# Kernel tuning notes

Measured on AMD Instinct MI355X. Metric: run time of the kernel, lower is better.

The kernel has to match this reference:

```python
import jax, jax.numpy as jnp
import numpy as np

N = 50000      # nodes
E = 800000     # edges (avg degree 16)
H = 128        # hidden_dim
GDIM = 64      # global feature dim
G = 10         # DiffGroupNorm groups
LAMDA = 0.01
EPS = 1e-5


def setup_inputs() -> dict:
    key = jax.random.key(0)
    ks = jax.random.split(key, 24)
    s = 0.05
    inp = {
        "x": jax.random.normal(ks[0], (N, H), dtype=jnp.float32),
        "edge_index": jax.random.randint(ks[1], (2, E), 0, N, dtype=jnp.int32),
        "edge_features": jax.random.normal(ks[2], (E, H), dtype=jnp.float32),
        "global_feat": jax.random.normal(ks[3], (1, GDIM), dtype=jnp.float32),
        # combine: Dense(H) on concat [x | messages | global] -> (H+H+GDIM, H)
        "Wc": jax.random.normal(ks[4], (H + H + GDIM, H), dtype=jnp.float32) * s,
        "bc": jnp.zeros((H,), jnp.float32),
    }
    for i, tag in enumerate(["a", "b"]):
        k = jax.random.split(ks[5 + i], 4)
        inp[f"W1{tag}"] = jax.random.normal(k[0], (H, H), dtype=jnp.float32) * s
        inp[f"b1{tag}"] = jnp.zeros((H,), jnp.float32)
        inp[f"W2{tag}"] = jax.random.normal(k[1], (H, H), dtype=jnp.float32) * s
        inp[f"b2{tag}"] = jnp.zeros((H,), jnp.float32)
        inp[f"linW{tag}"] = jax.random.normal(k[2], (H, G), dtype=jnp.float32) * s
        inp[f"linb{tag}"] = jnp.zeros((G,), jnp.float32)
        inp[f"gamma{tag}"] = jnp.ones((G * H,), jnp.float32)
        inp[f"beta{tag}"] = jnp.zeros((G * H,), jnp.float32)
    return inp


def _diff_group_norm(x, linW, linb, gamma, beta):
    # DiffGroupNorm: soft group assignment + per-(group,channel) batch norm.
    n, f = x.shape
    s = jax.nn.softmax(x @ linW + linb, axis=-1)            # [N, G]
    o = (s[:, :, None] * x[:, None, :]).reshape(n, G * f)   # [N, G*F]
    mu = o.mean(axis=0)
    var = o.var(axis=0)
    o = (o - mu) * jax.lax.rsqrt(var + EPS) * gamma + beta
    return x + LAMDA * o.reshape(n, G, f).sum(axis=1)


def _block(out, W1, b1, W2, b2, linW, linb, gamma, beta):
    h = jax.nn.softplus(out @ W1 + b1) @ W2 + b2
    h = _diff_group_norm(h, linW, linb, gamma, beta)
    return out + h


def reference(x, edge_index, edge_features, global_feat, Wc, bc,
              W1a, b1a, W2a, b2a, linWa, linba, gammaa, betaa,
              W1b, b1b, W2b, b2b, linWb, linbb, gammab, betab):
    n = x.shape[0]
    row = edge_index[0]
    # tf.scatter_nd accumulates duplicates -> segment sum over destination nodes
    messages = jax.ops.segment_sum(edge_features, row, num_segments=n)
    g = jnp.repeat(global_feat, n // global_feat.shape[0], axis=0)
    combined = jnp.concatenate([x, messages, g], axis=-1)
    out = jax.nn.softplus(combined @ Wc + bc)
    initial = out
    out = _block(out, W1a, b1a, W2a, b2a, linWa, linba, gammaa, betaa)
    out = _block(out, W1b, b1b, W2b, b2b, linWb, linbb, gammab, betab)
    return out + initial
```

## Files before the change

kernel.cpp:

```cpp
#include <hip/hip_runtime.h>
#include <math.h>

constexpr int NN = 50000;
constexpr int NE = 800000;
constexpr int HD = 128;
constexpr int NG = 10;
constexpr float LAM = 0.01f;
constexpr float EPSV = 1e-5f;
constexpr int NBLK = (NN + 255) / 256;
constexpr int GBLK = (NN + 63) / 64;
constexpr int NCOPY = 8;

typedef __attribute__((ext_vector_type(8))) short s8v;
typedef __attribute__((ext_vector_type(4))) float f4v;

constexpr int SMEM_BYTES = 76864;

__device__ __forceinline__ float softplus_f(float x) {
    return fmaxf(x, 0.f) + log1pf(expf(-fabsf(x)));
}
__device__ __forceinline__ unsigned short f2b(float f) {
    unsigned u = __float_as_uint(f);
    unsigned r = (u + 0x7FFFu + ((u >> 16) & 1u)) >> 16;
    return (unsigned short)r;
}
__device__ __forceinline__ float b2f(unsigned short u) {
    return __uint_as_float(((unsigned)u) << 16);
}

constexpr int EBLOCKS = (NE / 4 + 255) / 256;
__global__ __launch_bounds__(256) void hist_prep_kernel(
    const int* __restrict__ rows, int* __restrict__ cnt,
    const float* __restrict__ Wc,
    const float* __restrict__ W1a, const float* __restrict__ W2a,
    const float* __restrict__ W1b, const float* __restrict__ W2b,
    short* __restrict__ wct, short* __restrict__ wts)
{
    if ((int)blockIdx.x < EBLOCKS) {
        int base = (blockIdx.x * 256 + threadIdx.x) * 4;
        if (base < NE) {
            int4 r = *reinterpret_cast<const int4*>(rows + base);
            atomicAdd(&cnt[r.x], 1);
            atomicAdd(&cnt[r.y], 1);
            atomicAdd(&cnt[r.z], 1);
            atomicAdd(&cnt[r.w], 1);
        }
    } else {
        int i = (blockIdx.x - EBLOCKS) * 256 + threadIdx.x;
        if (i < 40960) {
            int n = i / 320, kk = i % 320;
            wct[i] = (short)f2b(Wc[kk * 128 + n]);
        } else if (i < 40960 + 4 * 16384) {
            int j = i - 40960;
            int mat = j >> 14;
            int idx = j & 16383;
            int n = idx >> 7, kk = idx & 127;
            const float* src = (mat == 0) ? W1a : (mat == 1) ? W2a
                             : (mat == 2) ? W1b : W2b;
            wts[j] = (short)f2b(src[kk * 128 + n]);
        }
    }
}

__global__ __launch_bounds__(256) void scan1_kernel(
    const int* __restrict__ cnt, int* __restrict__ bsum)
{
    __shared__ int red[256];
    int t = threadIdx.x;
    int i = blockIdx.x * 256 + t;
    red[t] = (i < NN) ? cnt[i] : 0;
    __syncthreads();
    for (int d = 128; d > 0; d >>= 1) {
        if (t < d) red[t] += red[t + d];
        __syncthreads();
    }
    if (t == 0) bsum[blockIdx.x] = red[0];
}

__global__ __launch_bounds__(256) void scan3_kernel(
    const int* __restrict__ cnt, const int* __restrict__ bsum,
    int* __restrict__ off, int* __restrict__ cur)
{
    __shared__ int sh[256];
    __shared__ int bs[256];
    __shared__ int basev;
    int t = threadIdx.x;
    int i = blockIdx.x * 256 + t;
    int v  = (i < NN) ? cnt[i] : 0;
    int bv = (t < NBLK) ? bsum[t] : 0;
    sh[t] = v; bs[t] = bv;
    __syncthreads();
    for (int d = 1; d < 256; d <<= 1) {
        int u1 = (t >= d) ? sh[t - d] : 0;
        int u2 = (t >= d) ? bs[t - d] : 0;
        __syncthreads();
        sh[t] += u1; bs[t] += u2;
        __syncthreads();
    }
    if (t == (int)blockIdx.x) basev = bs[t] - bv;
    __syncthreads();
    int excl = sh[t] - v + basev;
    if (i < NN) { off[i] = excl; cur[i] = excl; }
    if (i == NN - 1) off[NN] = NE;
}

__global__ __launch_bounds__(256) void fill_kernel(
    const int* __restrict__ rows, int* __restrict__ cur, int* __restrict__ eid)
{
    int base = (blockIdx.x * 256 + threadIdx.x) * 4;
    if (base < NE) {
        int4 r = *reinterpret_cast<const int4*>(rows + base);
        eid[atomicAdd(&cur[r.x], 1)] = base + 0;
        eid[atomicAdd(&cur[r.y], 1)] = base + 1;
        eid[atomicAdd(&cur[r.z], 1)] = base + 2;
        eid[atomicAdd(&cur[r.w], 1)] = base + 3;
    }
}

__global__ __launch_bounds__(256) void gather_kernel(
    const float* __restrict__ ef, const int* __restrict__ off,
    const int* __restrict__ eid, uint4* __restrict__ msgbf)
{
    int node = blockIdx.x * 4 + (threadIdx.x >> 6);
    if (node >= NN) return;
    int lane = threadIdx.x & 63;
    int eg = lane >> 4;
    int lc = lane & 15;
    int b = off[node], e = off[node + 1];
    float acc[8];
    #pragma unroll
    for (int j = 0; j < 8; ++j) acc[j] = 0.f;
    for (int i = b + eg; i < e; i += 4) {
        int ed = eid[i];
        const float* src = ef + (size_t)ed * HD + lc * 8;
        float4 v0 = *reinterpret_cast<const float4*>(src);
        float4 v1 = *reinterpret_cast<const float4*>(src + 4);
        acc[0] += v0.x; acc[1] += v0.y; acc[2] += v0.z; acc[3] += v0.w;
        acc[4] += v1.x; acc[5] += v1.y; acc[6] += v1.z; acc[7] += v1.w;
    }
    #pragma unroll
    for (int j = 0; j < 8; ++j) {
        acc[j] += __shfl_xor(acc[j], 16);
        acc[j] += __shfl_xor(acc[j], 32);
    }
    if (eg == 0) {
        uint4 pk;
        pk.x = (unsigned)f2b(acc[0]) | ((unsigned)f2b(acc[1]) << 16);
        pk.y = (unsigned)f2b(acc[2]) | ((unsigned)f2b(acc[3]) << 16);
        pk.z = (unsigned)f2b(acc[4]) | ((unsigned)f2b(acc[5]) << 16);
        pk.w = (unsigned)f2b(acc[6]) | ((unsigned)f2b(acc[7]) << 16);
        msgbf[(size_t)node * 16 + lc] = pk;
    }
}

__device__ __forceinline__ void fused12_tail(
    char* smem, const short* __restrict__ w2t,
    unsigned short* __restrict__ hbf, float* __restrict__ sout,
    float* __restrict__ sums_base, int m0)
{
    short* As = (short*)(smem);
    short* Ws = (short*)(smem + 17408);
    short* Ts = (short*)(smem + 52224);
    float* b1s = (float*)(smem + 69632);
    float* b2s = (float*)(smem + 70144);
    float* lws = (float*)(smem + 70656);
    float* lbs = (float*)(smem + 76288);
    float* hF = (float*)(smem);
    float* sS = (float*)(smem + 33792);

    const int tid = threadIdx.x;
    const int lane = tid & 63;
    const int wv = tid >> 6;
    const int fr = lane & 15;
    const int fc = lane >> 4;

    f4v acc[8];
    #pragma unroll
    for (int ct = 0; ct < 8; ++ct) acc[ct] = (f4v){0.f, 0.f, 0.f, 0.f};
    {
        const short* ap = As + (wv * 16 + fr) * 136 + fc * 8;
        const short* bp = Ws + fr * 136 + fc * 8;
        #pragma unroll
        for (int ks = 0; ks < 4; ++ks) {
            s8v a = *(const s8v*)(ap + ks * 32);
            #pragma unroll
            for (int ct = 0; ct < 8; ++ct) {
                s8v b = *(const s8v*)(bp + ct * 16 * 136 + ks * 32);
                acc[ct] = __builtin_amdgcn_mfma_f32_16x16x32_bf16(a, b, acc[ct], 0, 0, 0);
            }
        }
    }
    {
        int rb = wv * 16 + fc * 4;
        #pragma unroll
        for (int ct = 0; ct < 8; ++ct) {
            int col = ct * 16 + fr;
            float bv = b1s[col];
            #pragma unroll
            for (int r = 0; r < 4; ++r)
                Ts[(rb + r) * 136 + col] = (short)f2b(softplus_f(acc[ct][r] + bv));
        }
    }
    __syncthreads();
    {
        int col = tid >> 1, seg = (tid & 1) * 64;
        const short* src = w2t + (size_t)col * 128 + seg;
        #pragma unroll
        for (int j = 0; j < 8; ++j)
            *(s8v*)&Ws[col * 136 + seg + 8 * j] = *(const s8v*)(src + 8 * j);
    }
    __syncthreads();

    #pragma unroll
    for (int ct = 0; ct < 8; ++ct) acc[ct] = (f4v){0.f, 0.f, 0.f, 0.f};
    {
        const short* ap = Ts + (wv * 16 + fr) * 136 + fc * 8;
        const short* bp = Ws + fr * 136 + fc * 8;
        #pragma unroll
        for (int ks = 0; ks < 4; ++ks) {
            s8v a = *(const s8v*)(ap + ks * 32);
            #pragma unroll
            for (int ct = 0; ct < 8; ++ct) {
                s8v b = *(const s8v*)(bp + ct * 16 * 136 + ks * 32);
                acc[ct] = __builtin_amdgcn_mfma_f32_16x16x32_bf16(a, b, acc[ct], 0, 0, 0);
            }
        }
    }
    #pragma unroll
    for (int ct = 0; ct < 8; ++ct) {
        float bv = b2s[ct * 16 + fr];
        #pragma unroll
        for (int r = 0; r < 4; ++r) acc[ct][r] += bv;
    }
    float dot[4][10];
    #pragma unroll
    for (int r = 0; r < 4; ++r)
        #pragma unroll
        for (int g = 0; g < 10; ++g) dot[r][g] = 0.f;
    #pragma unroll
    for (int ct = 0; ct < 8; ++ct) {
        #pragma unroll
        for (int g = 0; g < 10; ++g) {
            float lwv = lws[(ct * 16 + fr) * 11 + g];
            #pragma unroll
            for (int r = 0; r < 4; ++r) dot[r][g] += acc[ct][r] * lwv;
        }
    }
    #pragma unroll
    for (int r = 0; r < 4; ++r)
        #pragma unroll
        for (int g = 0; g < 10; ++g) {
            float v = dot[r][g];
            v += __shfl_xor(v, 1);
            v += __shfl_xor(v, 2);
            v += __shfl_xor(v, 4);
            v += __shfl_xor(v, 8);
            dot[r][g] = v + lbs[g];
        }
    #pragma unroll
    for (int r = 0; r < 4; ++r) {
        float m = dot[r][0];
        #pragma unroll
        for (int g = 1; g < 10; ++g) m = fmaxf(m, dot[r][g]);
        float sum = 0.f;
        #pragma unroll
        for (int g = 0; g < 10; ++g) { dot[r][g] = expf(dot[r][g] - m); sum += dot[r][g]; }
        float inv = 1.f / sum;
        #pragma unroll
        for (int g = 0; g < 10; ++g) dot[r][g] *= inv;
    }
    const int growb = m0 + wv * 16 + fc * 4;
    const int rlocb = wv * 16 + fc * 4;
    unsigned short hq[8][4];
    #pragma unroll
    for (int ct = 0; ct < 8; ++ct) {
        int col = ct * 16 + fr;
        #pragma unroll
        for (int r = 0; r < 4; ++r) {
            hq[ct][r] = f2b(acc[ct][r]);
            int row = growb + r;
            if (row < NN) hbf[(size_t)row * 128 + col] = hq[ct][r];
        }
    }
    if (fr < 10) {
        #pragma unroll
        for (int r = 0; r < 4; ++r) {
            int row = growb + r;
            if (row < NN) {
                float v = 0.f;
                #pragma unroll
                for (int g = 0; g < 10; ++g) v = (fr == g) ? dot[r][g] : v;
                sout[(size_t)row * 10 + fr] = v;
            }
        }
    }
    __syncthreads();
    #pragma unroll
    for (int ct = 0; ct < 8; ++ct) {
        int col = ct * 16 + fr;
        #pragma unroll
        for (int r = 0; r < 4; ++r) {
            bool valid = (growb + r) < NN;
            hF[(rlocb + r) * 132 + col] = valid ? b2f(hq[ct][r]) : 0.f;
        }
    }
    if (fr < 10) {
        #pragma unroll
        for (int r = 0; r < 4; ++r) {
            bool valid = (growb + r) < NN;
            float v = 0.f;
            #pragma unroll
            for (int g = 0; g < 10; ++g) v = (fr == g) ? dot[r][g] : v;
            sS[(rlocb + r) * 10 + fr] = valid ? v : 0.f;
        }
    }
    __syncthreads();
    {
        float* sums = sums_base + (size_t)(blockIdx.x & (NCOPY - 1)) * 2560;
        const int c = tid & 127;
        const int g0 = (tid >> 7) * 5;
        float a1[5], a2[5];
        #pragma unroll
        for (int q = 0; q < 5; ++q) { a1[q] = 0.f; a2[q] = 0.f; }
        for (int n = 0; n < 64; ++n) {
            float hv = hF[n * 132 + c];
            #pragma unroll
            for (int q = 0; q < 5; ++q) {
                float pv = sS[n * 10 + g0 + q] * hv;
                a1[q] += pv;
                a2[q] += pv * pv;
            }
        }
        #pragma unroll
        for (int q = 0; q < 5; ++q) {
            atomicAdd(&sums[(g0 + q) * 128 + c], a1[q]);
            atomicAdd(&sums[1280 + (g0 + q) * 128 + c], a2[q]);
        }
    }
}

__global__ __launch_bounds__(256) void combine_f12a_kernel(
    const float* __restrict__ x, const short* __restrict__ msgbf,
    const float* __restrict__ gf, const short* __restrict__ wct,
    const float* __restrict__ bc,
    const short* __restrict__ w1t, const short* __restrict__ w2t,
    const float* __restrict__ b1, const float* __restrict__ b2,
    const float* __restrict__ linW, const float* __restrict__ linb,
    unsigned short* __restrict__ out0bf, unsigned short* __restrict__ hbf,
    float* __restrict__ sout, float* __restrict__ sums)
{
    __shared__ __align__(16) char smem[SMEM_BYTES];
    short* cAs = (short*)(smem);
    short* cWs = (short*)(smem + 9216);
    short* As  = (short*)(smem);
    short* Ws  = (short*)(smem + 17408);
    float* b1s = (float*)(smem + 69632);
    float* b2s = (float*)(smem + 70144);
    float* lws = (float*)(smem + 70656);
    float* lbs = (float*)(smem + 76288);
    float* bcs = (float*)(smem + 76352);

    const int tid = threadIdx.x;
    const int m0 = blockIdx.x * 64;
    if (tid < 128) { bcs[tid] = bc[tid]; b1s[tid] = b1[tid]; b2s[tid] = b2[tid]; }
    for (int i = tid; i < 1280; i += 256) lws[(i / 10) * 11 + (i % 10)] = linW[i];
    if (tid < 10) lbs[tid] = linb[tid];
    const int lane = tid & 63;
    const int wv = tid >> 6;
    const int fr = lane & 15;
    const int fc = lane >> 4;

    f4v acc[8];
    #pragma unroll
    for (int ct = 0; ct < 8; ++ct) acc[ct] = (f4v){0.f, 0.f, 0.f, 0.f};

    const int arow = tid >> 2;
    const int aseg = (tid & 3) * 16;
    const int wcol = tid >> 1;
    const int wseg = (tid & 1) * 32;

    for (int c = 0; c < 5; ++c) {
        const int k0 = c * 64;
        {
            short tmp[16];
            int grow = m0 + arow;
            if (grow >= NN) {
                #pragma unroll
                for (int j = 0; j < 16; ++j) tmp[j] = 0;
            } else if (c < 2) {
                const float* src = x + (size_t)grow * 128 + k0 + aseg;
                #pragma unroll
                for (int q = 0; q < 4; ++q) {
                    float4 v = *reinterpret_cast<const float4*>(src + 4 * q);
                    tmp[4*q+0] = (short)f2b(v.x); tmp[4*q+1] = (short)f2b(v.y);
                    tmp[4*q+2] = (short)f2b(v.z); tmp[4*q+3] = (short)f2b(v.w);
                }
            } else if (c < 4) {
                const short* src = msgbf + (size_t)grow * 128 + (k0 - 128) + aseg;
                *(s8v*)tmp = *(const s8v*)src;
                *(s8v*)(tmp + 8) = *(const s8v*)(src + 8);
            } else {
                const float* src = gf + aseg;
                #pragma unroll
                for (int q = 0; q < 4; ++q) {
                    float4 v = *reinterpret_cast<const float4*>(src + 4 * q);
                    tmp[4*q+0] = (short)f2b(v.x); tmp[4*q+1] = (short)f2b(v.y);
                    tmp[4*q+2] = (short)f2b(v.z); tmp[4*q+3] = (short)f2b(v.w);
                }
            }
            *(s8v*)&cAs[arow * 72 + aseg] = *(s8v*)tmp;
            *(s8v*)&cAs[arow * 72 + aseg + 8] = *(s8v*)(tmp + 8);
        }
        {
            const short* src = wct + (size_t)wcol * 320 + k0 + wseg;
            #pragma unroll
            for (int j = 0; j < 4; ++j)
                *(s8v*)&cWs[wcol * 72 + wseg + 8 * j] = *(const s8v*)(src + 8 * j);
        }
        __syncthreads();
        const short* ap = cAs + (wv * 16 + fr) * 72 + fc * 8;
        const short* bp = cWs + fr * 72 + fc * 8;
        #pragma unroll
        for (int ks = 0; ks < 2; ++ks) {
            s8v a = *(const s8v*)(ap + ks * 32);
            #pragma unroll
            for (int ct = 0; ct < 8; ++ct) {
                s8v b = *(const s8v*)(bp + ct * 16 * 72 + ks * 32);
                acc[ct] = __builtin_amdgcn_mfma_f32_16x16x32_bf16(a, b, acc[ct], 0, 0, 0);
            }
        }
        __syncthreads();
    }
    const int rbase = m0 + wv * 16 + fc * 4;
    const int rloc  = wv * 16 + fc * 4;
    #pragma unroll
    for (int ct = 0; ct < 8; ++ct) {
        int col = ct * 16 + fr;
        float bv = bcs[col];
        #pragma unroll
        for (int r = 0; r < 4; ++r) {
            unsigned short q = f2b(softplus_f(acc[ct][r] + bv));
            bool valid = (rbase + r) < NN;
            if (valid) out0bf[(size_t)(rbase + r) * 128 + col] = q;
            As[(rloc + r) * 136 + col] = valid ? (short)q : (short)0;
        }
    }
    {
        int col = tid >> 1, seg = (tid & 1) * 64;
        const short* src = w1t + (size_t)col * 128 + seg;
        #pragma unroll
        for (int j = 0; j < 8; ++j)
            *(s8v*)&Ws[col * 136 + seg + 8 * j] = *(const s8v*)(src + 8 * j);
    }
    __syncthreads();
    fused12_tail(smem, w2t, hbf, sout, sums, m0);
}

__global__ __launch_bounds__(256) void apply_f12b_kernel(
    const unsigned short* __restrict__ out0bf,
    const float* __restrict__ sums_a,
    const float* __restrict__ gamma_a, const float* __restrict__ beta_a,
    const short* __restrict__ w1t, const short* __restrict__ w2t,
    const float* __restrict__ b1, const float* __restrict__ b2,
    const float* __restrict__ linW, const float* __restrict__ linb,
    unsigned short* __restrict__ out1bf,
    unsigned short* __restrict__ hbf,
    float* __restrict__ sout,
    float* __restrict__ sums_b)
{
    __shared__ __align__(16) char smem[SMEM_BYTES];
    float* ws_  = (float*)(smem);
    float* mus_ = (float*)(smem + 5120);
    float* ks_  = (float*)(smem + 10240);
    float* ss_  = (float*)(smem + 10752);
    short* As   = (short*)(smem);
    short* Ws   = (short*)(smem + 17408);
    float* b1s  = (float*)(smem + 69632);
    float* b2s  = (float*)(smem + 70144);
    float* lws  = (float*)(smem + 70656);
    float* lbs  = (float*)(smem + 76288);

    const int tid = threadIdx.x;
    const int m0 = blockIdx.x * 64;
    if (tid < 128) { b1s[tid] = b1[tid]; b2s[tid] = b2[tid]; }
    for (int i = tid; i < 1280; i += 256) lws[(i / 10) * 11 + (i % 10)] = linW[i];
    if (tid < 10) lbs[tid] = linb[tid];
    const float invn = 1.f / (float)NN;
    for (int idx = tid; idx < 1280; idx += 256) {
        float s1 = 0.f, s2 = 0.f;
        #pragma unroll
        for (int k = 0; k < NCOPY; ++k) {
            s1 += sums_a[(size_t)k * 2560 + idx];
            s2 += sums_a[(size_t)k * 2560 + idx + 1280];
        }
        float mu = s1 * invn;
        float var = s2 * invn - mu * mu;
        float wg = rsqrtf(var + EPSV) * gamma_a[idx];
        ws_[idx] = wg;
        mus_[idx] = mu;
    }
    for (int i = tid; i < 640; i += 256) {
        int n = m0 + i / 10;
        ss_[i] = (n < NN) ? sout[(size_t)n * 10 + i % 10] : 0.f;
    }
    {
        int col = tid >> 1, seg = (tid & 1) * 64;
        const short* src = w1t + (size_t)col * 128 + seg;
        #pragma unroll
        for (int j = 0; j < 8; ++j)
            *(s8v*)&Ws[col * 136 + seg + 8 * j] = *(const s8v*)(src + 8 * j);
    }
    __syncthreads();
    if (tid < 128) {
        float kacc = 0.f;
        #pragma unroll
        for (int g = 0; g < NG; ++g) {
            int idx = g * 128 + tid;
            kacc += beta_a[idx] - mus_[idx] * ws_[idx];
        }
        ks_[tid] = kacc;
    }
    __syncthreads();
    const int tc = tid & 31, rg = tid >> 5;
    ushort4 vals[8];
    #pragma unroll
    for (int p = 0; p < 8; ++p) {
        int nl = p * 8 + rg;
        int n = m0 + nl;
        if (n >= NN) { vals[p].x = vals[p].y = vals[p].z = vals[p].w = 0; continue; }
        float A0 = 0.f, A1 = 0.f, A2 = 0.f, A3 = 0.f;
        #pragma unroll
        for (int g = 0; g < 10; ++g) {
            float sv = ss_[nl * 10 + g];
            float4 wv4 = *reinterpret_cast<const float4*>(&ws_[g * 128 + tc * 4]);
            A0 += sv * wv4.x; A1 += sv * wv4.y; A2 += sv * wv4.z; A3 += sv * wv4.w;
        }
        ushort4 hv4 = *reinterpret_cast<const ushort4*>(hbf + (size_t)n * 128 + tc * 4);
        ushort4 ov4 = *reinterpret_cast<const ushort4*>(out0bf + (size_t)n * 128 + tc * 4);
        float h0 = b2f(hv4.x), h1 = b2f(hv4.y), h2 = b2f(hv4.z), h3 = b2f(hv4.w);
        float r0 = b2f(ov4.x) + h0 + LAM * (h0 * A0 + ks_[tc * 4 + 0]);
        float r1 = b2f(ov4.y) + h1 + LAM * (h1 * A1 + ks_[tc * 4 + 1]);
        float r2 = b2f(ov4.z) + h2 + LAM * (h2 * A2 + ks_[tc * 4 + 2]);
        float r3 = b2f(ov4.w) + h3 + LAM * (h3 * A3 + ks_[tc * 4 + 3]);
        ushort4 o;
        o.x = f2b(r0); o.y = f2b(r1); o.z = f2b(r2); o.w = f2b(r3);
        *reinterpret_cast<ushort4*>(out1bf + (size_t)n * 128 + tc * 4) = o;
        vals[p] = o;
    }
    __syncthreads();
    #pragma unroll
    for (int p = 0; p < 8; ++p) {
        int row = p * 8 + rg;
        *reinterpret_cast<ushort4*>(&As[row * 136 + tc * 4]) = vals[p];
    }
    __syncthreads();
    fused12_tail(smem, w2t, hbf, sout, sums_b, m0);
}

__global__ __launch_bounds__(256) void apply_last_kernel(
    const unsigned short* __restrict__ out1bf,
    const unsigned short* __restrict__ hbf,
    const float* __restrict__ s, const float* __restrict__ sums,
    const float* __restrict__ gamma, const float* __restrict__ beta,
    const unsigned short* __restrict__ out0bf,
    float* __restrict__ dstf)
{
    __shared__ __align__(16) float ws_[1280];
    __shared__ float mus_[1280];
    __shared__ float ks_[128];
    __shared__ float ss_[640];
    const int tid = threadIdx.x;
    const int m0 = blockIdx.x * 64;
    const float invn = 1.f / (float)NN;
    for (int idx = tid; idx < 1280; idx += 256) {
        float s1 = 0.f, s2 = 0.f;
        #pragma unroll
        for (int k = 0; k < NCOPY; ++k) {
            s1 += sums[(size_t)k * 2560 + idx];
            s2 += sums[(size_t)k * 2560 + idx + 1280];
        }
        float mu = s1 * invn;
        float var = s2 * invn - mu * mu;
        float wg = rsqrtf(var + EPSV) * gamma[idx];
        ws_[idx] = wg;
        mus_[idx] = mu;
    }
    for (int i = tid; i < 640; i += 256) {
        int n = m0 + i / 10;
        ss_[i] = (n < NN) ? s[(size_t)n * 10 + i % 10] : 0.f;
    }
    __syncthreads();
    if (tid < 128) {
        float kacc = 0.f;
        #pragma unroll
        for (int g = 0; g < NG; ++g) {
            int idx = g * 128 + tid;
            kacc += beta[idx] - mus_[idx] * ws_[idx];
        }
        ks_[tid] = kacc;
    }
    __syncthreads();
    const int tc = tid & 31, rg = tid >> 5;
    #pragma unroll
    for (int p = 0; p < 8; ++p) {
        int nl = p * 8 + rg;
        int n = m0 + nl;
        if (n >= NN) continue;
        float A0 = 0.f, A1 = 0.f, A2 = 0.f, A3 = 0.f;
        #pragma unroll
        for (int g = 0; g < 10; ++g) {
            float sv = ss_[nl * 10 + g];
            float4 wv4 = *reinterpret_cast<const float4*>(&ws_[g * 128 + tc * 4]);
            A0 += sv * wv4.x; A1 += sv * wv4.y; A2 += sv * wv4.z; A3 += sv * wv4.w;
        }
        ushort4 hv4 = *reinterpret_cast<const ushort4*>(hbf + (size_t)n * 128 + tc * 4);
        ushort4 ov4 = *reinterpret_cast<const ushort4*>(out1bf + (size_t)n * 128 + tc * 4);
        ushort4 iv4 = *reinterpret_cast<const ushort4*>(out0bf + (size_t)n * 128 + tc * 4);
        float h0 = b2f(hv4.x), h1 = b2f(hv4.y), h2 = b2f(hv4.z), h3 = b2f(hv4.w);
        float r0 = b2f(ov4.x) + h0 + LAM * (h0 * A0 + ks_[tc * 4 + 0]) + b2f(iv4.x);
        float r1 = b2f(ov4.y) + h1 + LAM * (h1 * A1 + ks_[tc * 4 + 1]) + b2f(iv4.y);
        float r2 = b2f(ov4.z) + h2 + LAM * (h2 * A2 + ks_[tc * 4 + 2]) + b2f(iv4.z);
        float r3 = b2f(ov4.w) + h3 + LAM * (h3 * A3 + ks_[tc * 4 + 3]) + b2f(iv4.w);
        *reinterpret_cast<float4*>(dstf + (size_t)n * 128 + tc * 4) =
            make_float4(r0, r1, r2, r3);
    }
}

extern "C" void kernel_launch(void* const* d_in, const int* in_sizes, int n_in,
                              void* d_out, int out_size, void* d_ws, size_t ws_size,
                              hipStream_t stream)
{
    const float* x    = (const float*)d_in[0];
    const int*   eidx = (const int*)  d_in[1];
    const float* ef   = (const float*)d_in[2];
    const float* gf   = (const float*)d_in[3];
    const float* Wc   = (const float*)d_in[4];
    const float* bc   = (const float*)d_in[5];

    float* p = (float*)d_ws;
    int*   cnt    = (int*)p;                      p += NN;
    float* sums_a = p;                            p += (size_t)NCOPY * 2560;
    float* sums_b = p;                            p += (size_t)NCOPY * 2560;
    unsigned short* msgbf  = (unsigned short*)p;  p += (size_t)NN * 64;
    unsigned short* out0bf = (unsigned short*)p;  p += (size_t)NN * 64;
    unsigned short* out1bf = (unsigned short*)p;  p += (size_t)NN * 64;
    unsigned short* hbf    = (unsigned short*)p;  p += (size_t)NN * 64;
    float* sbuf = p;                              p += (size_t)NN * 10;
    short* wct  = (short*)p;
    short* wts  = wct + 40960;

    int* off   = (int*)out1bf;
    int* cur   = off + NN + 1;
    int* bsum  = cur + NN;
    int* eid   = (int*)hbf;

    hipMemsetAsync(cnt, 0, sizeof(int) * (NN + 2 * NCOPY * 2560), stream);

    hist_prep_kernel<<<EBLOCKS + 416, 256, 0, stream>>>(
        eidx, cnt, Wc, (const float*)d_in[6], (const float*)d_in[8],
        (const float*)d_in[14], (const float*)d_in[16], wct, wts);

    scan1_kernel<<<NBLK, 256, 0, stream>>>(cnt, bsum);
    scan3_kernel<<<NBLK, 256, 0, stream>>>(cnt, bsum, off, cur);
    fill_kernel <<<EBLOCKS, 256, 0, stream>>>(eidx, cur, eid);
    gather_kernel<<<(NN + 3) / 4, 256, 0, stream>>>(ef, off, eid, (uint4*)msgbf);

    const short* w1ta = wts;
    const short* w2ta = wts + 16384;
    const short* w1tb = wts + 32768;
    const short* w2tb = wts + 49152;

    combine_f12a_kernel<<<GBLK, 256, 0, stream>>>(
        x, (const short*)msgbf, gf, wct, bc,
        w1ta, w2ta, (const float*)d_in[7], (const float*)d_in[9],
        (const float*)d_in[10], (const float*)d_in[11],
        out0bf, hbf, sbuf, sums_a);

    apply_f12b_kernel<<<GBLK, 256, 0, stream>>>(
        out0bf, sums_a, (const float*)d_in[12], (const float*)d_in[13],
        w1tb, w2tb, (const float*)d_in[15], (const float*)d_in[17],
        (const float*)d_in[18], (const float*)d_in[19],
        out1bf, hbf, sbuf, sums_b);

    apply_last_kernel<<<GBLK, 256, 0, stream>>>(
        out1bf, hbf, sbuf, sums_b, (const float*)d_in[20], (const float*)d_in[21],
        out0bf, (float*)d_out);
}
```

Measured before the change: 397.3 us.

## Merge CSR build and gather front-end into one cooperative kernel

```diff
diff --git a/kernel.cpp b/kernel.cpp
--- a/kernel.cpp
+++ b/kernel.cpp
@@ -1,5 +1,8 @@
 #include <hip/hip_runtime.h>
+#include <hip/hip_cooperative_groups.h>
 #include <math.h>
+
+namespace cg = cooperative_groups;
 
 constexpr int NN = 50000;
 constexpr int NE = 800000;
@@ -10,6 +13,7 @@
 constexpr int NBLK = (NN + 255) / 256;
 constexpr int GBLK = (NN + 63) / 64;
 constexpr int NCOPY = 8;
+constexpr int FGRID = 1024;
 
 typedef __attribute__((ext_vector_type(8))) short s8v;
 typedef __attribute__((ext_vector_type(4))) float f4v;
@@ -28,128 +32,128 @@
     return __uint_as_float(((unsigned)u) << 16);
 }
 
-constexpr int EBLOCKS = (NE / 4 + 255) / 256;
-__global__ __launch_bounds__(256) void hist_prep_kernel(
-    const int* __restrict__ rows, int* __restrict__ cnt,
+__global__ __launch_bounds__(256) void frontend_kernel(
+    const int* __restrict__ rows,
+    int* __restrict__ zbase, int zcount,
+    int* __restrict__ cnt, int* __restrict__ bsum,
+    int* __restrict__ off, int* __restrict__ cur, int* __restrict__ eid,
+    const float* __restrict__ ef, uint4* __restrict__ msgbf,
+    const float* __restrict__ x, unsigned short* __restrict__ xbf,
     const float* __restrict__ Wc,
     const float* __restrict__ W1a, const float* __restrict__ W2a,
     const float* __restrict__ W1b, const float* __restrict__ W2b,
     short* __restrict__ wct, short* __restrict__ wts)
 {
-    if ((int)blockIdx.x < EBLOCKS) {
-        int base = (blockIdx.x * 256 + threadIdx.x) * 4;
-        if (base < NE) {
-            int4 r = *reinterpret_cast<const int4*>(rows + base);
-            atomicAdd(&cnt[r.x], 1);
-            atomicAdd(&cnt[r.y], 1);
-            atomicAdd(&cnt[r.z], 1);
-            atomicAdd(&cnt[r.w], 1);
-        }
-    } else {
-        int i = (blockIdx.x - EBLOCKS) * 256 + threadIdx.x;
-        if (i < 40960) {
-            int n = i / 320, kk = i % 320;
-            wct[i] = (short)f2b(Wc[kk * 128 + n]);
-        } else if (i < 40960 + 4 * 16384) {
-            int j = i - 40960;
-            int mat = j >> 14;
-            int idx = j & 16383;
-            int n = idx >> 7, kk = idx & 127;
-            const float* src = (mat == 0) ? W1a : (mat == 1) ? W2a
-                             : (mat == 2) ? W1b : W2b;
-            wts[j] = (short)f2b(src[kk * 128 + n]);
-        }
-    }
-}
-
-__global__ __launch_bounds__(256) void scan1_kernel(
-    const int* __restrict__ cnt, int* __restrict__ bsum)
-{
-    __shared__ int red[256];
-    int t = threadIdx.x;
-    int i = blockIdx.x * 256 + t;
-    red[t] = (i < NN) ? cnt[i] : 0;
-    __syncthreads();
-    for (int d = 128; d > 0; d >>= 1) {
-        if (t < d) red[t] += red[t + d];
+    cg::grid_group grid = cg::this_grid();
+    __shared__ int sA[256];
+    __shared__ int sB[256];
+    __shared__ int basev;
+    const int t = threadIdx.x;
+    const int gtid = blockIdx.x * 256 + t;
+    const int nthr = gridDim.x * 256;
+
+    for (int i = gtid; i < zcount; i += nthr) zbase[i] = 0;
+    for (int i = gtid; i < 40960; i += nthr) {
+        int n = i / 320, kk = i % 320;
+        wct[i] = (short)f2b(Wc[kk * 128 + n]);
+    }
+    for (int j = gtid; j < 65536; j += nthr) {
+        int mat = j >> 14, idx = j & 16383;
+        int n = idx >> 7, kk = idx & 127;
+        const float* src = (mat == 0) ? W1a : (mat == 1) ? W2a
+                         : (mat == 2) ? W1b : W2b;
+        wts[j] = (short)f2b(src[kk * 128 + n]);
+    }
+    for (int i = gtid; i < NN * 32; i += nthr) {
+        float4 v = reinterpret_cast<const float4*>(x)[i];
+        ushort4 o;
+        o.x = f2b(v.x); o.y = f2b(v.y); o.z = f2b(v.z); o.w = f2b(v.w);
+        reinterpret_cast<ushort4*>(xbf)[i] = o;
+    }
+    grid.sync();
+
+    for (int i = gtid; i < NE / 4; i += nthr) {
+        int4 r = reinterpret_cast<const int4*>(rows)[i];
+        atomicAdd(&cnt[r.x], 1);
+        atomicAdd(&cnt[r.y], 1);
+        atomicAdd(&cnt[r.z], 1);
+        atomicAdd(&cnt[r.w], 1);
+    }
+    grid.sync();
+
+    if ((int)blockIdx.x < NBLK) {
+        int i = blockIdx.x * 256 + t;
+        sA[t] = (i < NN) ? cnt[i] : 0;
         __syncthreads();
-    }
-    if (t == 0) bsum[blockIdx.x] = red[0];
-}
-
-__global__ __launch_bounds__(256) void scan3_kernel(
-    const int* __restrict__ cnt, const int* __restrict__ bsum,
-    int* __restrict__ off, int* __restrict__ cur)
-{
-    __shared__ int sh[256];
-    __shared__ int bs[256];
-    __shared__ int basev;
-    int t = threadIdx.x;
-    int i = blockIdx.x * 256 + t;
-    int v  = (i < NN) ? cnt[i] : 0;
-    int bv = (t < NBLK) ? bsum[t] : 0;
-    sh[t] = v; bs[t] = bv;
-    __syncthreads();
-    for (int d = 1; d < 256; d <<= 1) {
-        int u1 = (t >= d) ? sh[t - d] : 0;
-        int u2 = (t >= d) ? bs[t - d] : 0;
+        for (int d = 128; d > 0; d >>= 1) {
+            if (t < d) sA[t] += sA[t + d];
+            __syncthreads();
+        }
+        if (t == 0) bsum[blockIdx.x] = sA[0];
+    }
+    grid.sync();
+
+    if ((int)blockIdx.x < NBLK) {
+        int i = blockIdx.x * 256 + t;
+        int v  = (i < NN) ? cnt[i] : 0;
+        int bv = (t < NBLK) ? bsum[t] : 0;
+        sA[t] = v; sB[t] = bv;
         __syncthreads();
-        sh[t] += u1; bs[t] += u2;
+        for (int d = 1; d < 256; d <<= 1) {
+            int u1 = (t >= d) ? sA[t - d] : 0;
+            int u2 = (t >= d) ? sB[t - d] : 0;
+            __syncthreads();
+            sA[t] += u1; sB[t] += u2;
+            __syncthreads();
+        }
+        if (t == (int)blockIdx.x) basev = sB[t] - bv;
         __syncthreads();
-    }
-    if (t == (int)blockIdx.x) basev = bs[t] - bv;
-    __syncthreads();
-    int excl = sh[t] - v + basev;
-    if (i < NN) { off[i] = excl; cur[i] = excl; }
-    if (i == NN - 1) off[NN] = NE;
-}
-
-__global__ __launch_bounds__(256) void fill_kernel(
-    const int* __restrict__ rows, int* __restrict__ cur, int* __restrict__ eid)
-{
-    int base = (blockIdx.x * 256 + threadIdx.x) * 4;
-    if (base < NE) {
-        int4 r = *reinterpret_cast<const int4*>(rows + base);
+        int excl = sA[t] - v + basev;
+        if (i < NN) { off[i] = excl; cur[i] = excl; }
+        if (i == NN - 1) off[NN] = NE;
+    }
+    grid.sync();
+
+    for (int i = gtid; i < NE / 4; i += nthr) {
+        int4 r = reinterpret_cast<const int4*>(rows)[i];
+        int base = i * 4;
         eid[atomicAdd(&cur[r.x], 1)] = base + 0;
         eid[atomicAdd(&cur[r.y], 1)] = base + 1;
         eid[atomicAdd(&cur[r.z], 1)] = base + 2;
         eid[atomicAdd(&cur[r.w], 1)] = base + 3;
     }
-}
-
-__global__ __launch_bounds__(256) void gather_kernel(
-    const float* __restrict__ ef, const int* __restrict__ off,
-    const int* __restrict__ eid, uint4* __restrict__ msgbf)
-{
-    int node = blockIdx.x * 4 + (threadIdx.x >> 6);
-    if (node >= NN) return;
-    int lane = threadIdx.x & 63;
-    int eg = lane >> 4;
-    int lc = lane & 15;
-    int b = off[node], e = off[node + 1];
-    float acc[8];
-    #pragma unroll
-    for (int j = 0; j < 8; ++j) acc[j] = 0.f;
-    for (int i = b + eg; i < e; i += 4) {
-        int ed = eid[i];
-        const float* src = ef + (size_t)ed * HD + lc * 8;
-        float4 v0 = *reinterpret_cast<const float4*>(src);
-        float4 v1 = *reinterpret_cast<const float4*>(src + 4);
-        acc[0] += v0.x; acc[1] += v0.y; acc[2] += v0.z; acc[3] += v0.w;
-        acc[4] += v1.x; acc[5] += v1.y; acc[6] += v1.z; acc[7] += v1.w;
-    }
-    #pragma unroll
-    for (int j = 0; j < 8; ++j) {
-        acc[j] += __shfl_xor(acc[j], 16);
-        acc[j] += __shfl_xor(acc[j], 32);
-    }
-    if (eg == 0) {
-        uint4 pk;
-        pk.x = (unsigned)f2b(acc[0]) | ((unsigned)f2b(acc[1]) << 16);
-        pk.y = (unsigned)f2b(acc[2]) | ((unsigned)f2b(acc[3]) << 16);
-        pk.z = (unsigned)f2b(acc[4]) | ((unsigned)f2b(acc[5]) << 16);
-        pk.w = (unsigned)f2b(acc[6]) | ((unsigned)f2b(acc[7]) << 16);
-        msgbf[(size_t)node * 16 + lc] = pk;
+    grid.sync();
+
+    const int wv = t >> 6, lane = t & 63;
+    const int eg = lane >> 4, lc = lane & 15;
+    for (int ng = blockIdx.x; ng * 4 < NN; ng += gridDim.x) {
+        int node = ng * 4 + wv;
+        if (node >= NN) continue;
+        int b = off[node], e = off[node + 1];
+        float acc[8];
+        #pragma unroll
+        for (int j = 0; j < 8; ++j) acc[j] = 0.f;
+        for (int i = b + eg; i < e; i += 4) {
+            int ed = eid[i];
+            const float* src = ef + (size_t)ed * HD + lc * 8;
+            float4 v0 = *reinterpret_cast<const float4*>(src);
+            float4 v1 = *reinterpret_cast<const float4*>(src + 4);
+            acc[0] += v0.x; acc[1] += v0.y; acc[2] += v0.z; acc[3] += v0.w;
+            acc[4] += v1.x; acc[5] += v1.y; acc[6] += v1.z; acc[7] += v1.w;
+        }
+        #pragma unroll
+        for (int j = 0; j < 8; ++j) {
+            acc[j] += __shfl_xor(acc[j], 16);
+            acc[j] += __shfl_xor(acc[j], 32);
+        }
+        if (eg == 0) {
+            uint4 pk;
+            pk.x = (unsigned)f2b(acc[0]) | ((unsigned)f2b(acc[1]) << 16);
+            pk.y = (unsigned)f2b(acc[2]) | ((unsigned)f2b(acc[3]) << 16);
+            pk.z = (unsigned)f2b(acc[4]) | ((unsigned)f2b(acc[5]) << 16);
+            pk.w = (unsigned)f2b(acc[6]) | ((unsigned)f2b(acc[7]) << 16);
+            msgbf[(size_t)node * 16 + lc] = pk;
+        }
     }
 }
 
@@ -340,7 +344,7 @@
 }
 
 __global__ __launch_bounds__(256) void combine_f12a_kernel(
-    const float* __restrict__ x, const short* __restrict__ msgbf,
+    const unsigned short* __restrict__ xbf, const short* __restrict__ msgbf,
     const float* __restrict__ gf, const short* __restrict__ wct,
     const float* __restrict__ bc,
     const short* __restrict__ w1t, const short* __restrict__ w2t,
@@ -388,13 +392,9 @@
                 #pragma unroll
                 for (int j = 0; j < 16; ++j) tmp[j] = 0;
             } else if (c < 2) {
-                const float* src = x + (size_t)grow * 128 + k0 + aseg;
-                #pragma unroll
-                for (int q = 0; q < 4; ++q) {
-                    float4 v = *reinterpret_cast<const float4*>(src + 4 * q);
-                    tmp[4*q+0] = (short)f2b(v.x); tmp[4*q+1] = (short)f2b(v.y);
-                    tmp[4*q+2] = (short)f2b(v.z); tmp[4*q+3] = (short)f2b(v.w);
-                }
+                const short* src = (const short*)xbf + (size_t)grow * 128 + k0 + aseg;
+                *(s8v*)tmp = *(const s8v*)src;
+                *(s8v*)(tmp + 8) = *(const s8v*)(src + 8);
             } else if (c < 4) {
                 const short* src = msgbf + (size_t)grow * 128 + (k0 - 128) + aseg;
                 *(s8v*)tmp = *(const s8v*)src;
@@ -645,6 +645,7 @@
     unsigned short* out0bf = (unsigned short*)p;  p += (size_t)NN * 64;
     unsigned short* out1bf = (unsigned short*)p;  p += (size_t)NN * 64;
     unsigned short* hbf    = (unsigned short*)p;  p += (size_t)NN * 64;
+    unsigned short* xbf    = (unsigned short*)p;  p += (size_t)NN * 64;
     float* sbuf = p;                              p += (size_t)NN * 10;
     short* wct  = (short*)p;
     short* wts  = wct + 40960;
@@ -654,16 +655,27 @@
     int* bsum  = cur + NN;
     int* eid   = (int*)hbf;
 
-    hipMemsetAsync(cnt, 0, sizeof(int) * (NN + 2 * NCOPY * 2560), stream);
-
-    hist_prep_kernel<<<EBLOCKS + 416, 256, 0, stream>>>(
-        eidx, cnt, Wc, (const float*)d_in[6], (const float*)d_in[8],
-        (const float*)d_in[14], (const float*)d_in[16], wct, wts);
-
-    scan1_kernel<<<NBLK, 256, 0, stream>>>(cnt, bsum);
-    scan3_kernel<<<NBLK, 256, 0, stream>>>(cnt, bsum, off, cur);
-    fill_kernel <<<EBLOCKS, 256, 0, stream>>>(eidx, cur, eid);
-    gather_kernel<<<(NN + 3) / 4, 256, 0, stream>>>(ef, off, eid, (uint4*)msgbf);
+    const int zcount = NN + 2 * NCOPY * 2560;
+
+    {
+        const int* rows = eidx;
+        int* zbase = cnt;
+        int zc = zcount;
+        uint4* msg4 = (uint4*)msgbf;
+        const float* W1a = (const float*)d_in[6];
+        const float* W2a = (const float*)d_in[8];
+        const float* W1b = (const float*)d_in[14];
+        const float* W2b = (const float*)d_in[16];
+        void* args[] = {
+            (void*)&rows, (void*)&zbase, (void*)&zc,
+            (void*)&cnt, (void*)&bsum, (void*)&off, (void*)&cur, (void*)&eid,
+            (void*)&ef, (void*)&msg4, (void*)&x, (void*)&xbf,
+            (void*)&Wc, (void*)&W1a, (void*)&W2a, (void*)&W1b, (void*)&W2b,
+            (void*)&wct, (void*)&wts
+        };
+        hipLaunchCooperativeKernel((void*)frontend_kernel, dim3(FGRID), dim3(256),
+                                   args, 0, stream);
+    }
 
     const short* w1ta = wts;
     const short* w2ta = wts + 16384;
@@ -671,7 +683,7 @@
     const short* w2tb = wts + 49152;
 
     combine_f12a_kernel<<<GBLK, 256, 0, stream>>>(
-        x, (const short*)msgbf, gf, wct, bc,
+        xbf, (const short*)msgbf, gf, wct, bc,
         w1ta, w2ta, (const float*)d_in[7], (const float*)d_in[9],
         (const float*)d_in[10], (const float*)d_in[11],
         out0bf, hbf, sbuf, sums_a);
```

Result: slower. 916.1 us (+130.6%).
